# Kernel tuning notes

Measured on AMD Instinct MI355X. Metric: run time of the kernel, lower is better.

Reference implementation:

```python
import jax, jax.numpy as jnp
import numpy as np

B, S, D, H = 4, 2048, 512, 8
DEPTH = D // H


def setup_inputs() -> dict:
    key = jax.random.key(0)
    ks = jax.random.split(key, 12)
    scale = 0.02
    inp = {
        "q": jax.random.normal(ks[0], (B, S, D), dtype=jnp.float32),
        "k": jax.random.normal(ks[1], (B, S, D), dtype=jnp.float32),
        "v": jax.random.normal(ks[2], (B, S, D), dtype=jnp.float32),
        "mask": jax.random.randint(ks[3], (B, S, S), 0, 2, dtype=jnp.int32),
        "wq": jax.random.normal(ks[4], (D, D), dtype=jnp.float32) * scale,
        "bq": jnp.zeros((D,), dtype=jnp.float32),
        "wk": jax.random.normal(ks[5], (D, D), dtype=jnp.float32) * scale,
        "bk": jnp.zeros((D,), dtype=jnp.float32),
        "wv": jax.random.normal(ks[6], (D, D), dtype=jnp.float32) * scale,
        "bv": jnp.zeros((D,), dtype=jnp.float32),
        "wo": jax.random.normal(ks[7], (D, D), dtype=jnp.float32) * scale,
        "bo": jnp.zeros((D,), dtype=jnp.float32),
    }
    return inp


def _split_heads(x):
    # [B, S, D] -> [B, H, S, depth]
    b, s, _ = x.shape
    return x.reshape(b, s, H, DEPTH).transpose(0, 2, 1, 3)


def reference(q, k, v, mask, wq, bq, wk, bk, wv, bv, wo, bo):
    qh = _split_heads(q @ wq + bq)
    kh = _split_heads(k @ wk + bk)
    vh = _split_heads(v @ wv + bv)
    # scaled dot-product attention with additive mask, materializing [B,H,S,S]
    scores = jnp.einsum("bhqd,bhkd->bhqk", qh, kh) / jnp.sqrt(
        jnp.asarray(DEPTH, jnp.float32)
    )
    scores = scores + mask[:, None, :, :].astype(jnp.float32) * (-1e9)
    w = jax.nn.softmax(scores, axis=-1)
    o = jnp.einsum("bhqk,bhkd->bhqd", w, vh)
    o = o.transpose(0, 2, 1, 3).reshape(q.shape[0], -1, D)  # [B, S, D]
    return o @ wo + bo
```

## Files before the change

### kernel.cpp

```cpp
#include <hip/hip_runtime.h>
#include <hip/hip_bf16.h>
#include <stdint.h>

#define B_ 4
#define S_ 2048
#define D_ 512
#define H_ 8

typedef __attribute__((ext_vector_type(8))) short short8;
typedef __attribute__((ext_vector_type(4))) short short4v;
typedef __attribute__((ext_vector_type(4))) float f32x4;
typedef __attribute__((ext_vector_type(4))) unsigned short u16x4;

#define MFMA16(a,b,c) __builtin_amdgcn_mfma_f32_16x16x32_bf16((a),(b),(c),0,0,0)

#if __has_builtin(__builtin_amdgcn_mfma_f32_16x16x16bf16_1k)
#define HAVE16K 1
#define MFMA16K(a,b,c) __builtin_amdgcn_mfma_f32_16x16x16bf16_1k((a),(b),(c),0,0,0)
#else
#define HAVE16K 0
#endif

#if __has_builtin(__builtin_amdgcn_sbfe)
#define SBFE1(v, off) ((uint32_t)__builtin_amdgcn_sbfe((int)(v), (off), 1))
#else
#define SBFE1(v, off) ((uint32_t)(((int32_t)((v) << (31-(off)))) >> 31))
#endif

__device__ __forceinline__ unsigned short f2bf(float f){
    return __builtin_bit_cast(unsigned short, __float2bfloat16(f));
}

__device__ __forceinline__ float maskf(float p, uint32_t keep){
    return __builtin_bit_cast(float, __builtin_bit_cast(uint32_t, p) & keep);
}

__device__ __forceinline__ float max3f(float a, float b, float c){
    float d;
    asm("v_max3_f32 %0, %1, %2, %3" : "=v"(d) : "v"(a), "v"(b), "v"(c));
    return d;
}

__device__ __forceinline__ void gload_lds16(const void* g, void* l){
    __builtin_amdgcn_global_load_lds((const __attribute__((address_space(1))) uint32_t*)g,
                                     (__attribute__((address_space(3))) uint32_t*)l, 16, 0, 0);
}

__global__ __launch_bounds__(256) void maskpack_kernel(const int* __restrict__ mask,
                                                       uint32_t* __restrict__ out)
{
    int idx = blockIdx.x*256 + threadIdx.x;
    const int4* p = (const int4*)(mask + (size_t)idx*32);
    uint32_t bits = 0;
    #pragma unroll
    for (int c=0;c<8;c++){
        int4 v = p[c];
        if (v.x) bits |= 1u << (c*4+0);
        if (v.y) bits |= 1u << (c*4+1);
        if (v.z) bits |= 1u << (c*4+2);
        if (v.w) bits |= 1u << (c*4+3);
    }
    out[idx] = bits;
}

__global__ __launch_bounds__(256) void wtrans_kernel(const float* __restrict__ wq,
                                                     const float* __restrict__ wk,
                                                     const float* __restrict__ wv,
                                                     const float* __restrict__ wo,
                                                     unsigned short* __restrict__ wt)
{
    int f = blockIdx.x*256 + threadIdx.x;
    int mat = f >> 18;
    int rem = f & 262143;
    const float* Wm = (mat==0)?wq:(mat==1)?wk:(mat==2)?wv:wo;
    int kk = rem >> 9, nn = rem & 511;
    wt[(size_t)mat*262144 + (size_t)nn*512 + kk] = f2bf(Wm[rem]);
}

__global__ __launch_bounds__(256) void proj_kernel(
    const float* __restrict__ q, const float* __restrict__ k, const float* __restrict__ v,
    const float* __restrict__ bq, const float* __restrict__ bk, const float* __restrict__ bv,
    const unsigned short* __restrict__ wt, unsigned short* __restrict__ outb)
{
    __shared__ uint8_t smem[16384];
    const int t = threadIdx.x, l = t&63, w = t>>6, g = l>>4, ln = l&15;
    const int z = blockIdx.z;
    const float* X = (z==0)? q : (z==1)? k : v;
    const float* bias = (z==0)? bq : (z==1)? bk : bv;
    const unsigned short* WTz = wt + (size_t)z*(D_*D_);
    unsigned short* out = outb + (size_t)z*((size_t)B_*H_*S_*64);
    const float scale = (z==0)? 0.18033688011112042f : 1.0f;
    const int m0 = blockIdx.x*128, n0 = blockIdx.y*128;
    uint8_t* As = smem; uint8_t* Bs = smem + 8192;
    const int RB = (w>>1)*64, CB = (w&1)*64;

    const f32x4 zz = {0.f,0.f,0.f,0.f};
    f32x4 acc[4][4];
    #pragma unroll
    for (int i=0;i<4;i++)
        #pragma unroll
        for (int j=0;j<4;j++) acc[i][j] = zz;

    for (int k0=0; k0<D_; k0+=32){
        __syncthreads();
        #pragma unroll
        for (int i=0;i<2;i++){
            int qc = w + i*4;
            int row = qc*16 + (l>>2);
            int colb = ((l&3)*16) ^ ((row&3)<<4);
            gload_lds16((const uint8_t*)WTz + (((size_t)(n0+row)*D_ + k0)<<1) + colb,
                        Bs + qc*1024);
        }
        #pragma unroll
        for (int i=0;i<2;i++){
            int c = t + i*256;
            int row = c>>2, cc = c&3;
            const float4* src = (const float4*)(X + (size_t)(m0+row)*D_ + k0 + cc*8);
            float4 u0 = src[0], u1 = src[1];
            uint32_t c0,c1,c2,c3;
            asm("v_cvt_pk_bf16_f32 %0, %1, %2" : "=v"(c0) : "v"(u0.x), "v"(u0.y));
            asm("v_cvt_pk_bf16_f32 %0, %1, %2" : "=v"(c1) : "v"(u0.z), "v"(u0.w));
            asm("v_cvt_pk_bf16_f32 %0, %1, %2" : "=v"(c2) : "v"(u1.x), "v"(u1.y));
            asm("v_cvt_pk_bf16_f32 %0, %1, %2" : "=v"(c3) : "v"(u1.z), "v"(u1.w));
            uint4 pk4; pk4.x=c0; pk4.y=c1; pk4.z=c2; pk4.w=c3;
            *(uint4*)(As + row*64 + ((cc*16) ^ ((row&3)<<4))) = pk4;
        }
        __syncthreads();
        short8 af[4], bfr[4];
        #pragma unroll
        for (int ai=0; ai<4; ai++){
            int row = RB + 16*ai + ln;
            af[ai] = *(const short8*)(As + row*64 + ((16*g) ^ ((row&3)<<4)));
        }
        #pragma unroll
        for (int bj=0; bj<4; bj++){
            int row = CB + 16*bj + ln;
            bfr[bj] = *(const short8*)(Bs + row*64 + ((16*g) ^ ((row&3)<<4)));
        }
        if (z == 2){
            #pragma unroll
            for (int ai=0; ai<4; ai++)
                #pragma unroll
                for (int bj=0; bj<4; bj++)
                    acc[ai][bj] = MFMA16(bfr[bj], af[ai], acc[ai][bj]);
        } else {
            #pragma unroll
            for (int ai=0; ai<4; ai++)
                #pragma unroll
                for (int bj=0; bj<4; bj++)
                    acc[ai][bj] = MFMA16(af[ai], bfr[bj], acc[ai][bj]);
        }
    }

    if (z == 2){
        #pragma unroll
        for (int bj=0; bj<4; bj++){
            #pragma unroll
            for (int ai=0; ai<4; ai++){
                int s = m0 + RB + 16*ai + ln;
                #pragma unroll
                for (int r=0;r<4;r++){
                    int gn = n0 + CB + 16*bj + 4*g + r;
                    float val = acc[ai][bj][r] + bias[gn];
                    out[((size_t)(s>>11)*D_ + gn)*S_ + (s&2047)] = f2bf(val);
                }
            }
        }
    } else {
        #pragma unroll
        for (int bj=0; bj<4; bj++){
            int gn = n0 + CB + 16*bj + ln;
            float bv2 = bias[gn];
            int h = gn >> 6, dep = gn & 63;
            #pragma unroll
            for (int ai=0; ai<4; ai++){
                #pragma unroll
                for (int r=0;r<4;r++){
                    int gm = m0 + RB + 16*ai + 4*g + r;
                    float val = (acc[ai][bj][r] + bv2) * scale;
                    size_t o = ((size_t)(gm>>11)*H_ + h)*((size_t)S_*64) + (size_t)(gm&2047)*64 + dep;
                    out[o] = f2bf(val);
                }
            }
        }
    }
}

__global__ __launch_bounds__(256, 4) void attn_kernel(
    const unsigned short* __restrict__ qb, const unsigned short* __restrict__ kb,
    const unsigned short* __restrict__ vtb, const uint32_t* __restrict__ mb,
    unsigned short* __restrict__ ao)
{
#if HAVE16K
    __shared__ uint8_t smem[32768];
#else
    __shared__ uint8_t smem[40960];
#endif
    const int t = threadIdx.x, l = t&63, w = t>>6, g = l>>4, ln = l&15;
    const int bh = blockIdx.y;
    const int b = bh >> 3;
    const int q0 = blockIdx.x * 64;
    const unsigned short* Q  = qb + (size_t)bh*((size_t)S_*64);
    const unsigned short* K  = kb + (size_t)bh*((size_t)S_*64);
    const unsigned short* VT = vtb + ((size_t)b*D_ + (bh&7)*64)*S_;

    const int qrow = q0 + 16*w + ln;
    const short8 qf0 = *(const short8*)(Q + (size_t)qrow*64 + 8*g);
    const short8 qf1 = *(const short8*)(Q + (size_t)qrow*64 + 8*g + 32);

    const int Msw = (ln&7)<<4;
    const int sw0 = (16*g) ^ Msw;
    const int sw1 = (16*g + 64) ^ Msw;
    uint8_t* kB0 = smem + ln*128 + sw0;
    uint8_t* kB1 = smem + ln*128 + sw1;
#if HAVE16K
    uint8_t* vB  = smem + 16384 + ln*128;
    const int vo0 = (8*g     ) ^ Msw;
    const int vo1 = (8*g + 32) ^ Msw;
    const int vo2 = (8*g + 64) ^ Msw;
    const int vo3 = (8*g + 96) ^ Msw;
#else
    uint8_t* Pw = smem + 32768 + w*2048;
    uint8_t* prd0 = Pw + ln*128 + sw0;
    uint8_t* prd1 = Pw + ln*128 + sw1;
#endif

    int krow0 = w*8 + (l>>3), krow1 = (w+4)*8 + (l>>3);
    int colb0 = ((l&7)*16) ^ ((krow0&7)<<4);
    int colb1 = ((l&7)*16) ^ ((krow1&7)<<4);
    int kof0 = krow0*128 + colb0,     kof1 = krow1*128 + colb1;
    int vof0 = krow0*(S_*2) + colb0,  vof1 = krow1*(S_*2) + colb1;
    const int ldo0 = w*1024, ldo1 = (w+4)*1024;

    const uint2* mptr = (const uint2*)(mb + ((size_t)b*S_ + qrow)*64);

    const f32x4 zz = {0.f,0.f,0.f,0.f};
    f32x4 O[4], O5 = zz;
    #pragma unroll
    for (int i=0;i<4;i++) O[i] = zz;
    float c = 0.f;

    const short4v onesv = {0x3F80,0x3F80,0x3F80,0x3F80};
#if !HAVE16K
    const short8 ones8 = {0x3F80,0x3F80,0x3F80,0x3F80,0x3F80,0x3F80,0x3F80,0x3F80};
#endif

    gload_lds16((const uint8_t*)K  + kof0, smem + ldo0);
    gload_lds16((const uint8_t*)K  + kof1, smem + ldo1);
    gload_lds16((const uint8_t*)VT + vof0, smem + 16384 + ldo0);
    gload_lds16((const uint8_t*)VT + vof1, smem + 16384 + ldo1);
    kof0 += 8192; kof1 += 8192; vof0 += 128; vof1 += 128;
    int curb = 0;
    uint2 mmc = mptr[0];

    for (int it=0; it<S_/64; ++it){
        __syncthreads();
        if (it < S_/64 - 1){
            int nx = curb ^ 8192;
            gload_lds16((const uint8_t*)K  + kof0, smem + nx + ldo0);
            gload_lds16((const uint8_t*)K  + kof1, smem + nx + ldo1);
            gload_lds16((const uint8_t*)VT + vof0, smem + 16384 + nx + ldo0);
            gload_lds16((const uint8_t*)VT + vof1, smem + 16384 + nx + ldo1);
            kof0 += 8192; kof1 += 8192; vof0 += 128; vof1 += 128;
        }
        uint2 mmn = mptr[(it+1)&31];
        const uint8_t* b0 = kB0 + curb;
        const uint8_t* b1 = kB1 + curb;

        f32x4 st[4];
        __builtin_amdgcn_s_setprio(1);
        #pragma unroll
        for (int t4=0;t4<4;t4++){
            short8 kf0 = *(const short8*)(b0 + 2048*t4);
            short8 kf1 = *(const short8*)(b1 + 2048*t4);
            st[t4] = MFMA16(kf0, qf0, zz);
            st[t4] = MFMA16(kf1, qf1, st[t4]);
        }
        __builtin_amdgcn_s_setprio(0);

        float m0a = max3f(st[0][0], st[0][1], st[0][2]);
        float m1a = max3f(st[0][3], st[1][0], st[1][1]);
        float m2a = max3f(st[1][2], st[1][3], st[2][0]);
        float m3a = max3f(st[2][1], st[2][2], st[2][3]);
        float m4a = max3f(st[3][0], st[3][1], st[3][2]);
        float lmax = fmaxf(max3f(m0a, m1a, m2a), max3f(m3a, m4a, st[3][3]));
        if (__builtin_expect(__any(lmax > c + 8.0f), 0)){
            float rm = lmax;
            rm = fmaxf(rm, __shfl_xor(rm, 16));
            rm = fmaxf(rm, __shfl_xor(rm, 32));
            float cnew = fmaxf(c, rm);
            float al = __builtin_amdgcn_exp2f(c - cnew);
            c = cnew;
            #pragma unroll
            for (int r=0;r<4;r++){
                float aO = __shfl(al, 4*g + r);
                #pragma unroll
                for (int db=0; db<4; db++) O[db][r] *= aO;
                O5[r] *= aO;
            }
        }

        uint32_t mi0 = (~mmc.x) >> (4*g);
        uint32_t mi1 = (~mmc.y) >> (4*g);
        short4v pa[4];
        auto genp = [&](float cc){
            #pragma unroll
            for (int t4=0;t4<4;t4++){
                uint32_t mi = (t4 >= 2) ? mi1 : mi0;
                const int base = (t4&1)*16;
                float p0 = maskf(__builtin_amdgcn_exp2f(st[t4][0] - cc), SBFE1(mi, base+0));
                float p1 = maskf(__builtin_amdgcn_exp2f(st[t4][1] - cc), SBFE1(mi, base+1));
                float p2 = maskf(__builtin_amdgcn_exp2f(st[t4][2] - cc), SBFE1(mi, base+2));
                float p3 = maskf(__builtin_amdgcn_exp2f(st[t4][3] - cc), SBFE1(mi, base+3));
                uint32_t lo, hi;
                asm("v_cvt_pk_bf16_f32 %0, %1, %2" : "=v"(lo) : "v"(p0), "v"(p1));
                asm("v_cvt_pk_bf16_f32 %0, %1, %2" : "=v"(hi) : "v"(p2), "v"(p3));
                uint2 u; u.x = lo; u.y = hi;
                pa[t4] = __builtin_bit_cast(short4v, u);
            }
        };
        if (__builtin_expect(__all(c == 0.0f), 1)) genp(0.0f); else genp(c);
        mmc = mmn;

#if HAVE16K
        __builtin_amdgcn_s_setprio(1);
        const uint8_t* vb = vB + curb;
        #pragma unroll
        for (int db=0; db<4; db++){
            short4v vf0 = *(const short4v*)(vb + 2048*db + vo0);
            short4v vf1 = *(const short4v*)(vb + 2048*db + vo1);
            short4v vf2 = *(const short4v*)(vb + 2048*db + vo2);
            short4v vf3 = *(const short4v*)(vb + 2048*db + vo3);
            O[db] = MFMA16K(pa[0], vf0, O[db]);
            O[db] = MFMA16K(pa[1], vf1, O[db]);
            O[db] = MFMA16K(pa[2], vf2, O[db]);
            O[db] = MFMA16K(pa[3], vf3, O[db]);
        }
        O5 = MFMA16K(pa[0], onesv, O5);
        O5 = MFMA16K(pa[1], onesv, O5);
        O5 = MFMA16K(pa[2], onesv, O5);
        O5 = MFMA16K(pa[3], onesv, O5);
        __builtin_amdgcn_s_setprio(0);
#else
        #pragma unroll
        for (int t4=0;t4<4;t4++){
            uint2 u = __builtin_bit_cast(uint2, pa[t4]);
            *(uint2*)(Pw + ln*128 + ((32*t4 + 8*g) ^ Msw)) = u;
        }
        asm volatile("s_waitcnt lgkmcnt(0)" ::: "memory");
        short8 pa0 = *(const short8*)prd0;
        short8 pa1 = *(const short8*)prd1;
        __builtin_amdgcn_s_setprio(1);
        #pragma unroll
        for (int db=0; db<4; db++){
            int dr = 16*db + ln;
            short8 vf0 = *(const short8*)(smem + 16384 + curb + dr*128 + ((16*g     ) ^ ((dr&7)<<4)));
            short8 vf1 = *(const short8*)(smem + 16384 + curb + dr*128 + ((16*g + 64) ^ ((dr&7)<<4)));
            O[db] = MFMA16(pa0, vf0, O[db]);
            O[db] = MFMA16(pa1, vf1, O[db]);
        }
        O5 = MFMA16(pa0, ones8, O5);
        O5 = MFMA16(pa1, ones8, O5);
        __builtin_amdgcn_s_setprio(0);
#endif
        curb ^= 8192;
    }

    #pragma unroll
    for (int r=0;r<4;r++){
        float inv = 1.0f / O5[r];
        int gm = b*S_ + q0 + 16*w + 4*g + r;
        #pragma unroll
        for (int db=0; db<4; db++){
            int col = (bh&7)*64 + 16*db + ln;
            ao[(size_t)gm*D_ + col] = f2bf(O[db][r]*inv);
        }
    }
}

__global__ __launch_bounds__(256) void outproj_kernel(
    const unsigned short* __restrict__ ao, const unsigned short* __restrict__ wt,
    const float* __restrict__ bo, float* __restrict__ out)
{
    __shared__ uint8_t smem[16384];
    const int t = threadIdx.x, l = t&63, w = t>>6, g = l>>4, ln = l&15;
    const unsigned short* WTz = wt + (size_t)3*(D_*D_);
    const int m0 = blockIdx.x*128, n0 = blockIdx.y*128;
    uint8_t* As = smem; uint8_t* Bs = smem + 8192;
    const int RB = (w>>1)*64, CB = (w&1)*64;

    const f32x4 zz = {0.f,0.f,0.f,0.f};
    f32x4 acc[4][4];
    #pragma unroll
    for (int i=0;i<4;i++)
        #pragma unroll
        for (int j=0;j<4;j++) acc[i][j] = zz;

    for (int k0=0; k0<D_; k0+=32){
        __syncthreads();
        #pragma unroll
        for (int i=0;i<2;i++){
            int qc = w + i*4;
            int row = qc*16 + (l>>2);
            int colb = ((l&3)*16) ^ ((row&3)<<4);
            gload_lds16((const uint8_t*)WTz + (((size_t)(n0+row)*D_ + k0)<<1) + colb,
                        Bs + qc*1024);
            gload_lds16((const uint8_t*)ao + (((size_t)(m0+row)*D_ + k0)<<1) + colb,
                        As + qc*1024);
        }
        __syncthreads();
        short8 af[4], bfr[4];
        #pragma unroll
        for (int ai=0; ai<4; ai++){
            int row = RB + 16*ai + ln;
            af[ai] = *(const short8*)(As + row*64 + ((16*g) ^ ((row&3)<<4)));
        }
        #pragma unroll
        for (int bj=0; bj<4; bj++){
            int row = CB + 16*bj + ln;
            bfr[bj] = *(const short8*)(Bs + row*64 + ((16*g) ^ ((row&3)<<4)));
        }
        #pragma unroll
        for (int ai=0; ai<4; ai++)
            #pragma unroll
            for (int bj=0; bj<4; bj++)
                acc[ai][bj] = MFMA16(af[ai], bfr[bj], acc[ai][bj]);
    }

    #pragma unroll
    for (int bj=0; bj<4; bj++){
        int gn = n0 + CB + 16*bj + ln;
        float bv2 = bo[gn];
        #pragma unroll
        for (int ai=0; ai<4; ai++){
            #pragma unroll
            for (int r=0;r<4;r++){
                int gm = m0 + RB + 16*ai + 4*g + r;
                out[(size_t)gm*D_ + gn] = acc[ai][bj][r] + bv2;
            }
        }
    }
}

extern "C" void kernel_launch(void* const* d_in, const int* in_sizes, int n_in,
                              void* d_out, int out_size, void* d_ws, size_t ws_size,
                              hipStream_t stream)
{
    const float* q  = (const float*)d_in[0];
    const float* k  = (const float*)d_in[1];
    const float* v  = (const float*)d_in[2];
    const int* mask = (const int*)d_in[3];
    const float* wq = (const float*)d_in[4];
    const float* bq = (const float*)d_in[5];
    const float* wk = (const float*)d_in[6];
    const float* bk = (const float*)d_in[7];
    const float* wv = (const float*)d_in[8];
    const float* bv = (const float*)d_in[9];
    const float* wo = (const float*)d_in[10];
    const float* bo = (const float*)d_in[11];

    uint8_t* ws = (uint8_t*)d_ws;
    unsigned short* qkvb = (unsigned short*)ws;
    unsigned short* ao   = (unsigned short*)(ws + 25165824);
    unsigned short* wt   = (unsigned short*)(ws + 33554432);
    uint32_t*       mb   = (uint32_t*)      (ws + 35651584);
    float* out = (float*)d_out;

    maskpack_kernel<<<dim3(2048), dim3(256), 0, stream>>>(mask, mb);
    wtrans_kernel<<<dim3(4096), dim3(256), 0, stream>>>(wq, wk, wv, wo, wt);
    proj_kernel<<<dim3(64,4,3), dim3(256), 0, stream>>>(q, k, v, bq, bk, bv, wt, qkvb);
    attn_kernel<<<dim3(32,32), dim3(256), 0, stream>>>(qkvb, qkvb + 4194304, qkvb + 8388608, mb, ao);
    outproj_kernel<<<dim3(64,4), dim3(256), 0, stream>>>(ao, wt, bo, out);
}
```

Baseline: 135.0 us.

## Process two query tiles per wave in attention and merge prep kernels

```diff
diff --git a/kernel.cpp b/kernel.cpp
--- a/kernel.cpp
+++ b/kernel.cpp
@@ -46,35 +46,34 @@
                                      (__attribute__((address_space(3))) uint32_t*)l, 16, 0, 0);
 }
 
-__global__ __launch_bounds__(256) void maskpack_kernel(const int* __restrict__ mask,
-                                                       uint32_t* __restrict__ out)
+__global__ __launch_bounds__(256) void prep_kernel(
+    const int* __restrict__ mask, uint32_t* __restrict__ mout,
+    const float* __restrict__ wq, const float* __restrict__ wk,
+    const float* __restrict__ wv, const float* __restrict__ wo,
+    unsigned short* __restrict__ wt)
 {
-    int idx = blockIdx.x*256 + threadIdx.x;
-    const int4* p = (const int4*)(mask + (size_t)idx*32);
-    uint32_t bits = 0;
-    #pragma unroll
-    for (int c=0;c<8;c++){
-        int4 v = p[c];
-        if (v.x) bits |= 1u << (c*4+0);
-        if (v.y) bits |= 1u << (c*4+1);
-        if (v.z) bits |= 1u << (c*4+2);
-        if (v.w) bits |= 1u << (c*4+3);
-    }
-    out[idx] = bits;
-}
-
-__global__ __launch_bounds__(256) void wtrans_kernel(const float* __restrict__ wq,
-                                                     const float* __restrict__ wk,
-                                                     const float* __restrict__ wv,
-                                                     const float* __restrict__ wo,
-                                                     unsigned short* __restrict__ wt)
-{
-    int f = blockIdx.x*256 + threadIdx.x;
-    int mat = f >> 18;
-    int rem = f & 262143;
-    const float* Wm = (mat==0)?wq:(mat==1)?wk:(mat==2)?wv:wo;
-    int kk = rem >> 9, nn = rem & 511;
-    wt[(size_t)mat*262144 + (size_t)nn*512 + kk] = f2bf(Wm[rem]);
+    int bid = blockIdx.x;
+    if (bid < 4096){
+        int f = bid*256 + threadIdx.x;
+        int mat = f >> 18;
+        int rem = f & 262143;
+        const float* Wm = (mat==0)?wq:(mat==1)?wk:(mat==2)?wv:wo;
+        int kk = rem >> 9, nn = rem & 511;
+        wt[(size_t)mat*262144 + (size_t)nn*512 + kk] = f2bf(Wm[rem]);
+    } else {
+        int idx = (bid-4096)*256 + threadIdx.x;
+        const int4* p = (const int4*)(mask + (size_t)idx*32);
+        uint32_t bits = 0;
+        #pragma unroll
+        for (int c=0;c<8;c++){
+            int4 v = p[c];
+            if (v.x) bits |= 1u << (c*4+0);
+            if (v.y) bits |= 1u << (c*4+1);
+            if (v.z) bits |= 1u << (c*4+2);
+            if (v.w) bits |= 1u << (c*4+3);
+        }
+        mout[idx] = bits;
+    }
 }
 
 __global__ __launch_bounds__(256) void proj_kernel(
@@ -186,27 +185,26 @@
     }
 }
 
-__global__ __launch_bounds__(256, 4) void attn_kernel(
+__global__ __launch_bounds__(256, 2) void attn_kernel(
     const unsigned short* __restrict__ qb, const unsigned short* __restrict__ kb,
     const unsigned short* __restrict__ vtb, const uint32_t* __restrict__ mb,
     unsigned short* __restrict__ ao)
 {
-#if HAVE16K
     __shared__ uint8_t smem[32768];
-#else
-    __shared__ uint8_t smem[40960];
-#endif
     const int t = threadIdx.x, l = t&63, w = t>>6, g = l>>4, ln = l&15;
     const int bh = blockIdx.y;
     const int b = bh >> 3;
-    const int q0 = blockIdx.x * 64;
+    const int q0 = blockIdx.x * 128;
     const unsigned short* Q  = qb + (size_t)bh*((size_t)S_*64);
     const unsigned short* K  = kb + (size_t)bh*((size_t)S_*64);
     const unsigned short* VT = vtb + ((size_t)b*D_ + (bh&7)*64)*S_;
 
-    const int qrow = q0 + 16*w + ln;
-    const short8 qf0 = *(const short8*)(Q + (size_t)qrow*64 + 8*g);
-    const short8 qf1 = *(const short8*)(Q + (size_t)qrow*64 + 8*g + 32);
+    const int qrowA = q0 + 32*w + ln;
+    const int qrowB = qrowA + 16;
+    const short8 qf0A = *(const short8*)(Q + (size_t)qrowA*64 + 8*g);
+    const short8 qf1A = *(const short8*)(Q + (size_t)qrowA*64 + 8*g + 32);
+    const short8 qf0B = *(const short8*)(Q + (size_t)qrowB*64 + 8*g);
+    const short8 qf1B = *(const short8*)(Q + (size_t)qrowB*64 + 8*g + 32);
 
     const int Msw = (ln&7)<<4;
     const int sw0 = (16*g) ^ Msw;
@@ -219,10 +217,6 @@
     const int vo1 = (8*g + 32) ^ Msw;
     const int vo2 = (8*g + 64) ^ Msw;
     const int vo3 = (8*g + 96) ^ Msw;
-#else
-    uint8_t* Pw = smem + 32768 + w*2048;
-    uint8_t* prd0 = Pw + ln*128 + sw0;
-    uint8_t* prd1 = Pw + ln*128 + sw1;
 #endif
 
     int krow0 = w*8 + (l>>3), krow1 = (w+4)*8 + (l>>3);
@@ -232,18 +226,16 @@
     int vof0 = krow0*(S_*2) + colb0,  vof1 = krow1*(S_*2) + colb1;
     const int ldo0 = w*1024, ldo1 = (w+4)*1024;
 
-    const uint2* mptr = (const uint2*)(mb + ((size_t)b*S_ + qrow)*64);
+    const uint2* mptrA = (const uint2*)(mb + ((size_t)b*S_ + qrowA)*64);
+    const uint2* mptrB = (const uint2*)(mb + ((size_t)b*S_ + qrowB)*64);
 
     const f32x4 zz = {0.f,0.f,0.f,0.f};
-    f32x4 O[4], O5 = zz;
+    f32x4 OA[4], OB[4], O5A = zz, O5B = zz;
     #pragma unroll
-    for (int i=0;i<4;i++) O[i] = zz;
-    float c = 0.f;
+    for (int i=0;i<4;i++){ OA[i] = zz; OB[i] = zz; }
+    float cA = 0.f, cB = 0.f;
 
     const short4v onesv = {0x3F80,0x3F80,0x3F80,0x3F80};
-#if !HAVE16K
-    const short8 ones8 = {0x3F80,0x3F80,0x3F80,0x3F80,0x3F80,0x3F80,0x3F80,0x3F80};
-#endif
 
     gload_lds16((const uint8_t*)K  + kof0, smem + ldo0);
     gload_lds16((const uint8_t*)K  + kof1, smem + ldo1);
@@ -251,7 +243,7 @@
     gload_lds16((const uint8_t*)VT + vof1, smem + 16384 + ldo1);
     kof0 += 8192; kof1 += 8192; vof0 += 128; vof1 += 128;
     int curb = 0;
-    uint2 mmc = mptr[0];
+    uint2 mmA = mptrA[0], mmB = mptrB[0];
 
     for (int it=0; it<S_/64; ++it){
         __syncthreads();
@@ -263,64 +255,97 @@
             gload_lds16((const uint8_t*)VT + vof1, smem + 16384 + nx + ldo1);
             kof0 += 8192; kof1 += 8192; vof0 += 128; vof1 += 128;
         }
-        uint2 mmn = mptr[(it+1)&31];
+        uint2 mnA = mptrA[(it+1)&31], mnB = mptrB[(it+1)&31];
         const uint8_t* b0 = kB0 + curb;
         const uint8_t* b1 = kB1 + curb;
 
-        f32x4 st[4];
+        f32x4 stA[4], stB[4];
         __builtin_amdgcn_s_setprio(1);
         #pragma unroll
         for (int t4=0;t4<4;t4++){
             short8 kf0 = *(const short8*)(b0 + 2048*t4);
             short8 kf1 = *(const short8*)(b1 + 2048*t4);
-            st[t4] = MFMA16(kf0, qf0, zz);
-            st[t4] = MFMA16(kf1, qf1, st[t4]);
+            stA[t4] = MFMA16(kf0, qf0A, zz);
+            stB[t4] = MFMA16(kf0, qf0B, zz);
+            stA[t4] = MFMA16(kf1, qf1A, stA[t4]);
+            stB[t4] = MFMA16(kf1, qf1B, stB[t4]);
         }
         __builtin_amdgcn_s_setprio(0);
 
-        float m0a = max3f(st[0][0], st[0][1], st[0][2]);
-        float m1a = max3f(st[0][3], st[1][0], st[1][1]);
-        float m2a = max3f(st[1][2], st[1][3], st[2][0]);
-        float m3a = max3f(st[2][1], st[2][2], st[2][3]);
-        float m4a = max3f(st[3][0], st[3][1], st[3][2]);
-        float lmax = fmaxf(max3f(m0a, m1a, m2a), max3f(m3a, m4a, st[3][3]));
-        if (__builtin_expect(__any(lmax > c + 8.0f), 0)){
-            float rm = lmax;
-            rm = fmaxf(rm, __shfl_xor(rm, 16));
-            rm = fmaxf(rm, __shfl_xor(rm, 32));
-            float cnew = fmaxf(c, rm);
-            float al = __builtin_amdgcn_exp2f(c - cnew);
-            c = cnew;
+        float a0 = max3f(stA[0][0], stA[0][1], stA[0][2]);
+        float a1 = max3f(stA[0][3], stA[1][0], stA[1][1]);
+        float a2 = max3f(stA[1][2], stA[1][3], stA[2][0]);
+        float a3 = max3f(stA[2][1], stA[2][2], stA[2][3]);
+        float a4 = max3f(stA[3][0], stA[3][1], stA[3][2]);
+        float lmaxA = fmaxf(max3f(a0,a1,a2), max3f(a3,a4,stA[3][3]));
+        float b0m = max3f(stB[0][0], stB[0][1], stB[0][2]);
+        float b1m = max3f(stB[0][3], stB[1][0], stB[1][1]);
+        float b2m = max3f(stB[1][2], stB[1][3], stB[2][0]);
+        float b3m = max3f(stB[2][1], stB[2][2], stB[2][3]);
+        float b4m = max3f(stB[3][0], stB[3][1], stB[3][2]);
+        float lmaxB = fmaxf(max3f(b0m,b1m,b2m), max3f(b3m,b4m,stB[3][3]));
+
+        if (__builtin_expect(__any(fmaxf(lmaxA - cA, lmaxB - cB) > 8.0f), 0)){
+            float rmA = lmaxA;
+            rmA = fmaxf(rmA, __shfl_xor(rmA, 16));
+            rmA = fmaxf(rmA, __shfl_xor(rmA, 32));
+            float cAn = fmaxf(cA, rmA);
+            float alA = __builtin_amdgcn_exp2f(cA - cAn);
+            cA = cAn;
+            float rmB = lmaxB;
+            rmB = fmaxf(rmB, __shfl_xor(rmB, 16));
+            rmB = fmaxf(rmB, __shfl_xor(rmB, 32));
+            float cBn = fmaxf(cB, rmB);
+            float alB = __builtin_amdgcn_exp2f(cB - cBn);
+            cB = cBn;
             #pragma unroll
             for (int r=0;r<4;r++){
-                float aO = __shfl(al, 4*g + r);
+                float aO = __shfl(alA, 4*g + r);
+                float bO = __shfl(alB, 4*g + r);
                 #pragma unroll
-                for (int db=0; db<4; db++) O[db][r] *= aO;
-                O5[r] *= aO;
-            }
-        }
-
-        uint32_t mi0 = (~mmc.x) >> (4*g);
-        uint32_t mi1 = (~mmc.y) >> (4*g);
-        short4v pa[4];
-        auto genp = [&](float cc){
+                for (int db=0; db<4; db++){ OA[db][r] *= aO; OB[db][r] *= bO; }
+                O5A[r] *= aO; O5B[r] *= bO;
+            }
+        }
+
+        short4v paA[4], paB[4];
+        {
+            uint32_t mi0 = (~mmA.x) >> (4*g);
+            uint32_t mi1 = (~mmA.y) >> (4*g);
             #pragma unroll
             for (int t4=0;t4<4;t4++){
                 uint32_t mi = (t4 >= 2) ? mi1 : mi0;
                 const int base = (t4&1)*16;
-                float p0 = maskf(__builtin_amdgcn_exp2f(st[t4][0] - cc), SBFE1(mi, base+0));
-                float p1 = maskf(__builtin_amdgcn_exp2f(st[t4][1] - cc), SBFE1(mi, base+1));
-                float p2 = maskf(__builtin_amdgcn_exp2f(st[t4][2] - cc), SBFE1(mi, base+2));
-                float p3 = maskf(__builtin_amdgcn_exp2f(st[t4][3] - cc), SBFE1(mi, base+3));
+                float p0 = maskf(__builtin_amdgcn_exp2f(stA[t4][0] - cA), SBFE1(mi, base+0));
+                float p1 = maskf(__builtin_amdgcn_exp2f(stA[t4][1] - cA), SBFE1(mi, base+1));
+                float p2 = maskf(__builtin_amdgcn_exp2f(stA[t4][2] - cA), SBFE1(mi, base+2));
+                float p3 = maskf(__builtin_amdgcn_exp2f(stA[t4][3] - cA), SBFE1(mi, base+3));
                 uint32_t lo, hi;
                 asm("v_cvt_pk_bf16_f32 %0, %1, %2" : "=v"(lo) : "v"(p0), "v"(p1));
                 asm("v_cvt_pk_bf16_f32 %0, %1, %2" : "=v"(hi) : "v"(p2), "v"(p3));
                 uint2 u; u.x = lo; u.y = hi;
-                pa[t4] = __builtin_bit_cast(short4v, u);
-            }
-        };
-        if (__builtin_expect(__all(c == 0.0f), 1)) genp(0.0f); else genp(c);
-        mmc = mmn;
+                paA[t4] = __builtin_bit_cast(short4v, u);
+            }
+        }
+        {
+            uint32_t mi0 = (~mmB.x) >> (4*g);
+            uint32_t mi1 = (~mmB.y) >> (4*g);
+            #pragma unroll
+            for (int t4=0;t4<4;t4++){
+                uint32_t mi = (t4 >= 2) ? mi1 : mi0;
+                const int base = (t4&1)*16;
+                float p0 = maskf(__builtin_amdgcn_exp2f(stB[t4][0] - cB), SBFE1(mi, base+0));
+                float p1 = maskf(__builtin_amdgcn_exp2f(stB[t4][1] - cB), SBFE1(mi, base+1));
+                float p2 = maskf(__builtin_amdgcn_exp2f(stB[t4][2] - cB), SBFE1(mi, base+2));
+                float p3 = maskf(__builtin_amdgcn_exp2f(stB[t4][3] - cB), SBFE1(mi, base+3));
+                uint32_t lo, hi;
+                asm("v_cvt_pk_bf16_f32 %0, %1, %2" : "=v"(lo) : "v"(p0), "v"(p1));
+                asm("v_cvt_pk_bf16_f32 %0, %1, %2" : "=v"(hi) : "v"(p2), "v"(p3));
+                uint2 u; u.x = lo; u.y = hi;
+                paB[t4] = __builtin_bit_cast(short4v, u);
+            }
+        }
+        mmA = mnA; mmB = mnB;
 
 #if HAVE16K
         __builtin_amdgcn_s_setprio(1);
@@ -331,49 +356,37 @@
             short4v vf1 = *(const short4v*)(vb + 2048*db + vo1);
             short4v vf2 = *(const short4v*)(vb + 2048*db + vo2);
             short4v vf3 = *(const short4v*)(vb + 2048*db + vo3);
-            O[db] = MFMA16K(pa[0], vf0, O[db]);
-            O[db] = MFMA16K(pa[1], vf1, O[db]);
-            O[db] = MFMA16K(pa[2], vf2, O[db]);
-            O[db] = MFMA16K(pa[3], vf3, O[db]);
-        }
-        O5 = MFMA16K(pa[0], onesv, O5);
-        O5 = MFMA16K(pa[1], onesv, O5);
-        O5 = MFMA16K(pa[2], onesv, O5);
-        O5 = MFMA16K(pa[3], onesv, O5);
+            OA[db] = MFMA16K(paA[0], vf0, OA[db]);
+            OB[db] = MFMA16K(paB[0], vf0, OB[db]);
+            OA[db] = MFMA16K(paA[1], vf1, OA[db]);
+            OB[db] = MFMA16K(paB[1], vf1, OB[db]);
+            OA[db] = MFMA16K(paA[2], vf2, OA[db]);
+            OB[db] = MFMA16K(paB[2], vf2, OB[db]);
+            OA[db] = MFMA16K(paA[3], vf3, OA[db]);
+            OB[db] = MFMA16K(paB[3], vf3, OB[db]);
+        }
+        #pragma unroll
+        for (int t4=0;t4<4;t4++){
+            O5A = MFMA16K(paA[t4], onesv, O5A);
+            O5B = MFMA16K(paB[t4], onesv, O5B);
+        }
         __builtin_amdgcn_s_setprio(0);
 #else
-        #pragma unroll
-        for (int t4=0;t4<4;t4++){
-            uint2 u = __builtin_bit_cast(uint2, pa[t4]);
-            *(uint2*)(Pw + ln*128 + ((32*t4 + 8*g) ^ Msw)) = u;
-        }
-        asm volatile("s_waitcnt lgkmcnt(0)" ::: "memory");
-        short8 pa0 = *(const short8*)prd0;
-        short8 pa1 = *(const short8*)prd1;
-        __builtin_amdgcn_s_setprio(1);
-        #pragma unroll
-        for (int db=0; db<4; db++){
-            int dr = 16*db + ln;
-            short8 vf0 = *(const short8*)(smem + 16384 + curb + dr*128 + ((16*g     ) ^ ((dr&7)<<4)));
-            short8 vf1 = *(const short8*)(smem + 16384 + curb + dr*128 + ((16*g + 64) ^ ((dr&7)<<4)));
-            O[db] = MFMA16(pa0, vf0, O[db]);
-            O[db] = MFMA16(pa1, vf1, O[db]);
-        }
-        O5 = MFMA16(pa0, ones8, O5);
-        O5 = MFMA16(pa1, ones8, O5);
-        __builtin_amdgcn_s_setprio(0);
 #endif
         curb ^= 8192;
     }
 
     #pragma unroll
     for (int r=0;r<4;r++){
-        float inv = 1.0f / O5[r];
-        int gm = b*S_ + q0 + 16*w + 4*g + r;
+        float invA = 1.0f / O5A[r];
+        float invB = 1.0f / O5B[r];
+        int gmA = b*S_ + q0 + 32*w + 4*g + r;
+        int gmB = gmA + 16;
         #pragma unroll
         for (int db=0; db<4; db++){
             int col = (bh&7)*64 + 16*db + ln;
-            ao[(size_t)gm*D_ + col] = f2bf(O[db][r]*inv);
+            ao[(size_t)gmA*D_ + col] = f2bf(OA[db][r]*invA);
+            ao[(size_t)gmB*D_ + col] = f2bf(OB[db][r]*invB);
         }
     }
 }
@@ -466,9 +479,8 @@
     uint32_t*       mb   = (uint32_t*)      (ws + 35651584);
     float* out = (float*)d_out;
 
-    maskpack_kernel<<<dim3(2048), dim3(256), 0, stream>>>(mask, mb);
-    wtrans_kernel<<<dim3(4096), dim3(256), 0, stream>>>(wq, wk, wv, wo, wt);
+    prep_kernel<<<dim3(6144), dim3(256), 0, stream>>>(mask, mb, wq, wk, wv, wo, wt);
     proj_kernel<<<dim3(64,4,3), dim3(256), 0, stream>>>(q, k, v, bq, bk, bv, wt, qkvb);
-    attn_kernel<<<dim3(32,32), dim3(256), 0, stream>>>(qkvb, qkvb + 4194304, qkvb + 8388608, mb, ao);
+    attn_kernel<<<dim3(16,32), dim3(256), 0, stream>>>(qkvb, qkvb + 4194304, qkvb + 8388608, mb, ao);
     outproj_kernel<<<dim3(64,4), dim3(256), 0, stream>>>(ao, wt, bo, out);
 }
```

New measurement: 134.8 us. About the same (-0.1%).
